# Optimization experiments

Hardware: AMD Instinct MI355X
Metric: run time of the kernel (lower is better)

The kernel has to match this reference:

```python
import jax, jax.numpy as jnp
import numpy as np

N_NODES = 50000
N_EDGES = 800000
D = 128
ALPHA = 0.2  # LeakyReLU negative slope


def setup_inputs() -> dict:
    key = jax.random.key(0)
    k1, k2, k3, k4 = jax.random.split(key, 4)
    inputs = jax.random.normal(k1, (N_NODES, D), dtype=jnp.float32)
    edge = jax.random.randint(k2, (2, N_EDGES), 0, N_NODES, dtype=jnp.int64)
    # xavier_normal with gain=1.414 as in the torch module
    std_W = 1.414 * np.sqrt(2.0 / (D + D))
    W = jax.random.normal(k3, (D, D), dtype=jnp.float32) * std_W
    std_a = 1.414 * np.sqrt(2.0 / (1 + D))
    a = jax.random.normal(k4, (1, D), dtype=jnp.float32) * std_a
    return {"inputs": inputs, "edge": edge, "W": W, "a": a}


def reference(inputs, edge, W, a):
    # h = inputs @ W  (shared projection; note concat([W,W],0) applied to
    # [x_src || x_dst] is exactly h[src] + h[dst])
    h = inputs @ W                                   # [N, D]
    src, dst = edge[0], edge[1]
    s = h[src] + h[dst]                              # [E, D] gathered edge features
    s = jnp.where(s > 0, s, ALPHA * s)               # LeakyReLU
    edge_e = jnp.exp(s @ a[0])                       # [E] unnormalized attention
    n = inputs.shape[0]
    # sparse.mm(coo, ones) -> per-row sum of edge_e; duplicates summed (coalesce)
    e_rowsum = jax.ops.segment_sum(edge_e, src, num_segments=n)        # [N]
    # sparse.mm(coo, h) -> sum_j edge_e * h[dst]
    h_prime = jax.ops.segment_sum(edge_e[:, None] * h[dst], src, num_segments=n)  # [N, D]
    h_prime = h_prime / e_rowsum[:, None]
    return jax.nn.relu(h_prime)  # concat=True path
```

## Files before the change

### kernel.cpp

```cpp
#include <hip/hip_runtime.h>
#include <cstdint>
#include <cstddef>

#define D 128
#define ALPHA 0.2f

typedef _Float16 half8_t __attribute__((ext_vector_type(8)));
typedef _Float16 v2h __attribute__((ext_vector_type(2)));
typedef __attribute__((ext_vector_type(4))) float f32x4_t;

static __device__ __forceinline__ ushort f2h(float f) {
    _Float16 h = (_Float16)f;
    return *(ushort*)&h;
}

static __device__ __forceinline__ float dot2f(v2h x, v2h y, float c) {
#if __has_builtin(__builtin_amdgcn_fdot2)
    return __builtin_amdgcn_fdot2(x, y, c, false);
#else
    return fmaf((float)x[0], (float)y[0], fmaf((float)x[1], (float)y[1], c));
#endif
}

__global__ __launch_bounds__(256) void prep_kernel(const float* __restrict__ W,
                                                   const float* __restrict__ a,
                                                   ushort* __restrict__ Wt,
                                                   ushort* __restrict__ Ah,
                                                   int* __restrict__ counts, int N) {
    int idx = blockIdx.x * 256 + threadIdx.x;
    if (idx < 16384) {
        int k = idx >> 7;
        int n = idx & 127;
        Wt[n * 128 + k] = f2h(W[idx]);
    }
    if (idx < 128) Ah[idx] = f2h(a[idx]);
    if (idx < N) counts[idx] = 0;
}

__global__ __launch_bounds__(256) void gemm_h_kernel(const float* __restrict__ A,
                                                     const ushort* __restrict__ Wt,
                                                     ushort* __restrict__ Hf,
                                                     int N) {
    __shared__ ushort Alds[64][136];
    const int tid = threadIdx.x;
    const int r0 = blockIdx.x * 64;

#pragma unroll
    for (int it = 0; it < 8; ++it) {
        int idx = it * 256 + tid;
        int r = idx >> 5;
        int c4 = (idx & 31) * 4;
        float4 v = make_float4(0.f, 0.f, 0.f, 0.f);
        if (r0 + r < N) v = *(const float4*)(A + (size_t)(r0 + r) * D + c4);
        ushort4 b;
        b.x = f2h(v.x); b.y = f2h(v.y); b.z = f2h(v.z); b.w = f2h(v.w);
        *(ushort4*)&Alds[r][c4] = b;
    }
    __syncthreads();

    const int lane = tid & 63;
    const int w = tid >> 6;
    const int wm = w >> 1;
    const int wn = w & 1;
    const int l15 = lane & 15;
    const int koff = (lane >> 4) * 8;

    f32x4_t acc[2][4];
#pragma unroll
    for (int mt = 0; mt < 2; ++mt)
#pragma unroll
        for (int nt = 0; nt < 4; ++nt) acc[mt][nt] = (f32x4_t){0.f, 0.f, 0.f, 0.f};

    const int arow = wm * 32 + l15;
#pragma unroll
    for (int kk = 0; kk < 4; ++kk) {
        half8_t am0 = *(const half8_t*)&Alds[arow][kk * 32 + koff];
        half8_t am1 = *(const half8_t*)&Alds[arow + 16][kk * 32 + koff];
        half8_t bn[4];
#pragma unroll
        for (int nt = 0; nt < 4; ++nt)
            bn[nt] = *(const half8_t*)(Wt + (size_t)(wn * 64 + nt * 16 + l15) * 128 + kk * 32 + koff);
#pragma unroll
        for (int nt = 0; nt < 4; ++nt) {
            acc[0][nt] = __builtin_amdgcn_mfma_f32_16x16x32_f16(am0, bn[nt], acc[0][nt], 0, 0, 0);
            acc[1][nt] = __builtin_amdgcn_mfma_f32_16x16x32_f16(am1, bn[nt], acc[1][nt], 0, 0, 0);
        }
    }

    const int crow = (lane >> 4) * 4;
#pragma unroll
    for (int mt = 0; mt < 2; ++mt)
#pragma unroll
        for (int nt = 0; nt < 4; ++nt)
#pragma unroll
            for (int r = 0; r < 4; ++r) {
                int row = r0 + wm * 32 + mt * 16 + crow + r;
                if (row < N)
                    Hf[(size_t)row * D + wn * 64 + nt * 16 + l15] = f2h(acc[mt][nt][r]);
            }
}

__global__ __launch_bounds__(256) void hist_rank_kernel(const int* __restrict__ src,
                                                        int* __restrict__ counts,
                                                        int* __restrict__ rank, int E) {
    int i = blockIdx.x * 256 + threadIdx.x;
    if (i >= E) return;
    rank[i] = atomicAdd(&counts[src[i]], 1);
}

__global__ __launch_bounds__(256) void scan_partial_kernel(const int* __restrict__ counts,
                                                           int* __restrict__ blocksum, int N) {
    __shared__ int wsum[4];
    int tid = threadIdx.x;
    int i = blockIdx.x * 256 + tid;
    int x = (i < N) ? counts[i] : 0;
#pragma unroll
    for (int off = 32; off > 0; off >>= 1) x += __shfl_down(x, off);
    if ((tid & 63) == 0) wsum[tid >> 6] = x;
    __syncthreads();
    if (tid == 0) blocksum[blockIdx.x] = wsum[0] + wsum[1] + wsum[2] + wsum[3];
}

__global__ __launch_bounds__(256) void scan_final_kernel(const int* __restrict__ counts,
                                                         const int* __restrict__ blocksum,
                                                         int* __restrict__ starts,
                                                         int nblk, int N) {
    __shared__ int bsum[4];
    __shared__ int wsum[4];
    int tid = threadIdx.x;
    int lane = tid & 63, w = tid >> 6;

    int x0 = (tid < nblk && tid < (int)blockIdx.x) ? blocksum[tid] : 0;
#pragma unroll
    for (int off = 32; off > 0; off >>= 1) x0 += __shfl_down(x0, off);
    if (lane == 0) bsum[w] = x0;
    __syncthreads();
    int blkoff = bsum[0] + bsum[1] + bsum[2] + bsum[3];

    int i = blockIdx.x * 256 + tid;
    int c = (i < N) ? counts[i] : 0;
    int x = c;
#pragma unroll
    for (int off = 1; off < 64; off <<= 1) {
        int y = __shfl_up(x, off);
        if (lane >= off) x += y;
    }
    if (lane == 63) wsum[w] = x;
    __syncthreads();
    int woff = blkoff;
    for (int j = 0; j < w; ++j) woff += wsum[j];
    int pre = woff + x - c;
    if (i < N) {
        starts[i] = pre;
        if (i == N - 1) starts[N] = pre + c;
    }
}

__global__ __launch_bounds__(256) void scatter_kernel(const int* __restrict__ src,
                                                      const int* __restrict__ dst,
                                                      const int* __restrict__ rank,
                                                      const int* __restrict__ starts,
                                                      int* __restrict__ dsts_sorted, int E) {
    int i = blockIdx.x * 256 + threadIdx.x;
    if (i >= E) return;
    int pos = starts[src[i]] + rank[i];
    dsts_sorted[pos] = dst[i];
}

template <bool FULL>
__device__ __forceinline__ void process_chunk(const ushort* __restrict__ Hf,
                                              const int* __restrict__ dsts_sorted,
                                              int base, int cnt, int l,
                                              v2h hs2, v2h av2, v2h alpha2,
                                              float& acc0, float& acc1, float& rsp) {
    uint fu[16];
#pragma unroll
    for (int j = 0; j < 16; ++j) {
        int idx = FULL ? (base + j) : (base + (j < cnt ? j : 0));
        int dj = dsts_sorted[idx];
        const ushort* rp = Hf + ((size_t)(uint)dj << 7);
        fu[j] = *(const uint*)(rp + (l << 1));
    }
    float p[16];
#pragma unroll
    for (int j = 0; j < 16; ++j) {
        v2h hv = *(v2h*)&fu[j];
        v2h s = hs2 + hv;
        s = __builtin_elementwise_max(s, s * alpha2);
        float pj = dot2f(s, av2, 0.0f);
        p[j] = (FULL || j < cnt) ? pj : -1e30f;
    }
    {
        bool hi = l & 1;
#pragma unroll
        for (int i = 0; i < 8; ++i) {
            float send = hi ? p[i] : p[i + 8];
            float recv = __shfl_xor(send, 1);
            p[i] = (hi ? p[i + 8] : p[i]) + recv;
        }
        hi = l & 2;
#pragma unroll
        for (int i = 0; i < 4; ++i) {
            float send = hi ? p[i] : p[i + 4];
            float recv = __shfl_xor(send, 2);
            p[i] = (hi ? p[i + 4] : p[i]) + recv;
        }
        hi = l & 4;
#pragma unroll
        for (int i = 0; i < 2; ++i) {
            float send = hi ? p[i] : p[i + 2];
            float recv = __shfl_xor(send, 4);
            p[i] = (hi ? p[i + 2] : p[i]) + recv;
        }
        hi = l & 8;
        {
            float send = hi ? p[0] : p[1];
            float recv = __shfl_xor(send, 8);
            p[0] = (hi ? p[1] : p[0]) + recv;
        }
        p[0] += __shfl_xor(p[0], 16);
        p[0] += __shfl_xor(p[0], 32);
    }
    float e = __expf(p[0]);
    rsp += e;

    const int brev[16] = {0, 8, 4, 12, 2, 10, 6, 14, 1, 9, 5, 13, 3, 11, 7, 15};
#pragma unroll
    for (int j = 0; j < 16; ++j) {
        float ej = __uint_as_float(
            (uint)__builtin_amdgcn_readlane((int)__float_as_uint(e), brev[j]));
        v2h hv = *(v2h*)&fu[j];
        acc0 = fmaf((float)hv[0], ej, acc0);
        acc1 = fmaf((float)hv[1], ej, acc1);
    }
}

__global__ __launch_bounds__(64) void node_kernel(const ushort* __restrict__ Hf,
                                                  const int* __restrict__ starts,
                                                  const int* __restrict__ dsts_sorted,
                                                  const ushort* __restrict__ Ah,
                                                  float* __restrict__ out, int N) {
    const int node = blockIdx.x;
    const int l = threadIdx.x;

    const int beg = starts[node];
    const int end = starts[node + 1];

    uint hu = *(const uint*)(Hf + ((size_t)node << 7) + (l << 1));
    v2h hs2 = *(v2h*)&hu;
    uint au = *(const uint*)(Ah + (l << 1));
    v2h av2 = *(v2h*)&au;
    const v2h alpha2 = {(_Float16)ALPHA, (_Float16)ALPHA};

    float acc0 = 0.f, acc1 = 0.f, rsp = 0.f;

    int base = beg;
    for (; base + 16 <= end; base += 16)
        process_chunk<true>(Hf, dsts_sorted, base, 16, l, hs2, av2, alpha2, acc0, acc1, rsp);
    if (base < end)
        process_chunk<false>(Hf, dsts_sorted, base, end - base, l, hs2, av2, alpha2, acc0, acc1, rsp);

    float rs = rsp;
    rs += __shfl_xor(rs, 1);
    rs += __shfl_xor(rs, 2);
    rs += __shfl_xor(rs, 4);
    rs += __shfl_xor(rs, 8);

    float inv = 1.0f / rs;
    float2 o;
    o.x = fmaxf(acc0 * inv, 0.f);
    o.y = fmaxf(acc1 * inv, 0.f);
    *(float2*)(out + ((size_t)node << 7) + (l << 1)) = o;
}

extern "C" void kernel_launch(void* const* d_in, const int* in_sizes, int n_in,
                              void* d_out, int out_size, void* d_ws, size_t ws_size,
                              hipStream_t stream) {
    const float* inputs = (const float*)d_in[0];
    const int* edge = (const int*)d_in[1];
    const float* W = (const float*)d_in[2];
    const float* a = (const float*)d_in[3];
    float* out = (float*)d_out;

    const int N = in_sizes[0] / D;
    const int E = in_sizes[1] / 2;

    const int* src = edge;
    const int* dst = edge + E;

    ushort* wt = (ushort*)d_ws;
    ushort* ah = wt + 16384;
    ushort* hf = ah + 128;
    int* counts = (int*)(hf + (size_t)N * D);
    int* starts = counts + N;
    int* blocksum = starts + N + 1;
    int* rank = blocksum + 256;
    int* dsts_sorted = rank + E;

    const int nblk = (N + 255) / 256;
    const int eblk = (E + 255) / 256;

    prep_kernel<<<nblk, 256, 0, stream>>>(W, a, wt, ah, counts, N);
    gemm_h_kernel<<<(N + 63) / 64, 256, 0, stream>>>(inputs, wt, hf, N);
    hist_rank_kernel<<<eblk, 256, 0, stream>>>(src, counts, rank, E);
    scan_partial_kernel<<<nblk, 256, 0, stream>>>(counts, blocksum, N);
    scan_final_kernel<<<nblk, 256, 0, stream>>>(counts, blocksum, starts, nblk, N);
    scatter_kernel<<<eblk, 256, 0, stream>>>(src, dst, rank, starts, dsts_sorted, E);
    node_kernel<<<N, 64, 0, stream>>>(hf, starts, dsts_sorted, ah, out, N);
}
```

Before: 116.7 us.

## Merge scan passes, fold zeroing into GEMM, and double-load neighbor chunks

Several changes land together. The two-pass block scan becomes a single kernel where each block re-sums all earlier counts directly. Zeroing the counts array moves into the GEMM kernel, and the 'a' conversion moves into the node kernel, which shrinks the prep kernel to W only. The node kernel now issues loads for two 16-edge chunks before computing either, raising memory-level parallelism on the gathers at the cost of more registers. The single-pass scan does quadratic total reads of counts (about 196 blocks each reading up to 50K ints), which costs bandwidth but saves one launch.

```diff
diff --git a/kernel.cpp b/kernel.cpp
--- a/kernel.cpp
+++ b/kernel.cpp
@@ -22,25 +22,22 @@
 #endif
 }
 
-__global__ __launch_bounds__(256) void prep_kernel(const float* __restrict__ W,
-                                                   const float* __restrict__ a,
-                                                   ushort* __restrict__ Wt,
-                                                   ushort* __restrict__ Ah,
-                                                   int* __restrict__ counts, int N) {
+__global__ __launch_bounds__(256) void w_prep_kernel(const float* __restrict__ W,
+                                                     ushort* __restrict__ Wt) {
     int idx = blockIdx.x * 256 + threadIdx.x;
-    if (idx < 16384) {
-        int k = idx >> 7;
-        int n = idx & 127;
-        Wt[n * 128 + k] = f2h(W[idx]);
-    }
-    if (idx < 128) Ah[idx] = f2h(a[idx]);
-    if (idx < N) counts[idx] = 0;
+    int k = idx >> 7;
+    int n = idx & 127;
+    Wt[n * 128 + k] = f2h(W[idx]);
 }
 
 __global__ __launch_bounds__(256) void gemm_h_kernel(const float* __restrict__ A,
                                                      const ushort* __restrict__ Wt,
                                                      ushort* __restrict__ Hf,
+                                                     int* __restrict__ counts,
                                                      int N) {
+    int zi = blockIdx.x * 256 + threadIdx.x;
+    if (zi < N) counts[zi] = 0;
+
     __shared__ ushort Alds[64][136];
     const int tid = threadIdx.x;
     const int r0 = blockIdx.x * 64;
@@ -108,36 +105,23 @@
     rank[i] = atomicAdd(&counts[src[i]], 1);
 }
 
-__global__ __launch_bounds__(256) void scan_partial_kernel(const int* __restrict__ counts,
-                                                           int* __restrict__ blocksum, int N) {
-    __shared__ int wsum[4];
-    int tid = threadIdx.x;
-    int i = blockIdx.x * 256 + tid;
-    int x = (i < N) ? counts[i] : 0;
-#pragma unroll
-    for (int off = 32; off > 0; off >>= 1) x += __shfl_down(x, off);
-    if ((tid & 63) == 0) wsum[tid >> 6] = x;
-    __syncthreads();
-    if (tid == 0) blocksum[blockIdx.x] = wsum[0] + wsum[1] + wsum[2] + wsum[3];
-}
-
-__global__ __launch_bounds__(256) void scan_final_kernel(const int* __restrict__ counts,
-                                                         const int* __restrict__ blocksum,
-                                                         int* __restrict__ starts,
-                                                         int nblk, int N) {
+__global__ __launch_bounds__(256) void scan_kernel(const int* __restrict__ counts,
+                                                   int* __restrict__ starts, int N) {
     __shared__ int bsum[4];
     __shared__ int wsum[4];
     int tid = threadIdx.x;
     int lane = tid & 63, w = tid >> 6;
 
-    int x0 = (tid < nblk && tid < (int)blockIdx.x) ? blocksum[tid] : 0;
+    int lim = blockIdx.x << 8;
+    int x0 = 0;
+    for (int i = tid; i < lim; i += 256) x0 += counts[i];
 #pragma unroll
     for (int off = 32; off > 0; off >>= 1) x0 += __shfl_down(x0, off);
     if (lane == 0) bsum[w] = x0;
     __syncthreads();
     int blkoff = bsum[0] + bsum[1] + bsum[2] + bsum[3];
 
-    int i = blockIdx.x * 256 + tid;
+    int i = (blockIdx.x << 8) + tid;
     int c = (i < N) ? counts[i] : 0;
     int x = c;
 #pragma unroll
@@ -167,20 +151,21 @@
     dsts_sorted[pos] = dst[i];
 }
 
-template <bool FULL>
-__device__ __forceinline__ void process_chunk(const ushort* __restrict__ Hf,
-                                              const int* __restrict__ dsts_sorted,
-                                              int base, int cnt, int l,
-                                              v2h hs2, v2h av2, v2h alpha2,
-                                              float& acc0, float& acc1, float& rsp) {
-    uint fu[16];
+__device__ __forceinline__ void load_chunk16(const ushort* __restrict__ Hf,
+                                             const int* __restrict__ dsts_sorted,
+                                             int base, int l, uint fu[16]) {
 #pragma unroll
     for (int j = 0; j < 16; ++j) {
-        int idx = FULL ? (base + j) : (base + (j < cnt ? j : 0));
-        int dj = dsts_sorted[idx];
+        int dj = dsts_sorted[base + j];
         const ushort* rp = Hf + ((size_t)(uint)dj << 7);
         fu[j] = *(const uint*)(rp + (l << 1));
     }
+}
+
+template <bool FULL>
+__device__ __forceinline__ void compute_chunk16(const uint fu[16], int cnt, int l,
+                                                v2h hs2, v2h av2, v2h alpha2,
+                                                float& acc0, float& acc1, float& rsp) {
     float p[16];
 #pragma unroll
     for (int j = 0; j < 16; ++j) {
@@ -238,7 +223,7 @@
 __global__ __launch_bounds__(64) void node_kernel(const ushort* __restrict__ Hf,
                                                   const int* __restrict__ starts,
                                                   const int* __restrict__ dsts_sorted,
-                                                  const ushort* __restrict__ Ah,
+                                                  const float* __restrict__ a,
                                                   float* __restrict__ out, int N) {
     const int node = blockIdx.x;
     const int l = threadIdx.x;
@@ -248,17 +233,37 @@
 
     uint hu = *(const uint*)(Hf + ((size_t)node << 7) + (l << 1));
     v2h hs2 = *(v2h*)&hu;
-    uint au = *(const uint*)(Ah + (l << 1));
-    v2h av2 = *(v2h*)&au;
+    float2 af = ((const float2*)a)[l];
+    v2h av2 = {(_Float16)af.x, (_Float16)af.y};
     const v2h alpha2 = {(_Float16)ALPHA, (_Float16)ALPHA};
 
     float acc0 = 0.f, acc1 = 0.f, rsp = 0.f;
 
     int base = beg;
-    for (; base + 16 <= end; base += 16)
-        process_chunk<true>(Hf, dsts_sorted, base, 16, l, hs2, av2, alpha2, acc0, acc1, rsp);
-    if (base < end)
-        process_chunk<false>(Hf, dsts_sorted, base, end - base, l, hs2, av2, alpha2, acc0, acc1, rsp);
+    for (; base + 32 <= end; base += 32) {
+        uint fuA[16], fuB[16];
+        load_chunk16(Hf, dsts_sorted, base, l, fuA);
+        load_chunk16(Hf, dsts_sorted, base + 16, l, fuB);
+        compute_chunk16<true>(fuA, 16, l, hs2, av2, alpha2, acc0, acc1, rsp);
+        compute_chunk16<true>(fuB, 16, l, hs2, av2, alpha2, acc0, acc1, rsp);
+    }
+    if (base + 16 <= end) {
+        uint fu[16];
+        load_chunk16(Hf, dsts_sorted, base, l, fu);
+        compute_chunk16<true>(fu, 16, l, hs2, av2, alpha2, acc0, acc1, rsp);
+        base += 16;
+    }
+    if (base < end) {
+        int cnt = end - base;
+        uint fu[16];
+#pragma unroll
+        for (int j = 0; j < 16; ++j) {
+            int dj = dsts_sorted[base + (j < cnt ? j : 0)];
+            const ushort* rp = Hf + ((size_t)(uint)dj << 7);
+            fu[j] = *(const uint*)(rp + (l << 1));
+        }
+        compute_chunk16<false>(fu, cnt, l, hs2, av2, alpha2, acc0, acc1, rsp);
+    }
 
     float rs = rsp;
     rs += __shfl_xor(rs, 1);
@@ -289,22 +294,19 @@
     const int* dst = edge + E;
 
     ushort* wt = (ushort*)d_ws;
-    ushort* ah = wt + 16384;
-    ushort* hf = ah + 128;
+    ushort* hf = wt + 16384;
     int* counts = (int*)(hf + (size_t)N * D);
     int* starts = counts + N;
-    int* blocksum = starts + N + 1;
-    int* rank = blocksum + 256;
+    int* rank = starts + N + 1;
     int* dsts_sorted = rank + E;
 
     const int nblk = (N + 255) / 256;
     const int eblk = (E + 255) / 256;
 
-    prep_kernel<<<nblk, 256, 0, stream>>>(W, a, wt, ah, counts, N);
-    gemm_h_kernel<<<(N + 63) / 64, 256, 0, stream>>>(inputs, wt, hf, N);
+    w_prep_kernel<<<64, 256, 0, stream>>>(W, wt);
+    gemm_h_kernel<<<(N + 63) / 64, 256, 0, stream>>>(inputs, wt, hf, counts, N);
     hist_rank_kernel<<<eblk, 256, 0, stream>>>(src, counts, rank, E);
-    scan_partial_kernel<<<nblk, 256, 0, stream>>>(counts, blocksum, N);
-    scan_final_kernel<<<nblk, 256, 0, stream>>>(counts, blocksum, starts, nblk, N);
+    scan_kernel<<<nblk, 256, 0, stream>>>(counts, starts, N);
     scatter_kernel<<<eblk, 256, 0, stream>>>(src, dst, rank, starts, dsts_sorted, E);
-    node_kernel<<<N, 64, 0, stream>>>(hf, starts, dsts_sorted, ah, out, N);
-}
+    node_kernel<<<N, 64, 0, stream>>>(hf, starts, dsts_sorted, a, out, N);
+}
```

Result: slower. 147.5 us (+26.3%).

## Partition histogram and scatter by source range; use atomic cursors instead of rank array

Applied to the files above, without the earlier changes.

The histogram and scatter kernels now launch eight times as many blocks, and each group handles only edges whose source falls in one eighth of the node range. The apparent aim is to keep atomic targets local to one XCD/L2 slice. The per-edge rank array is dropped: the scatter kernel takes slots with atomic increments on a cursor array initialised from the scan. In exchange, every edge is read eight times in both kernels, and neighbour order within a row is no longer deterministic.

```diff
diff --git a/kernel.cpp b/kernel.cpp
--- a/kernel.cpp
+++ b/kernel.cpp
@@ -100,12 +100,17 @@
             }
 }
 
-__global__ __launch_bounds__(256) void hist_rank_kernel(const int* __restrict__ src,
-                                                        int* __restrict__ counts,
-                                                        int* __restrict__ rank, int E) {
-    int i = blockIdx.x * 256 + threadIdx.x;
+__global__ __launch_bounds__(256) void hist8_kernel(const int* __restrict__ src,
+                                                    int* __restrict__ counts,
+                                                    int E, int N) {
+    int b = blockIdx.x;
+    int g = b & 7;
+    int i = ((b >> 3) << 8) + threadIdx.x;
     if (i >= E) return;
-    rank[i] = atomicAdd(&counts[src[i]], 1);
+    int s = src[i];
+    int lo = (g * N) >> 3;
+    int hi = ((g + 1) * N) >> 3;
+    if (s >= lo && s < hi) atomicAdd(&counts[s], 1);
 }
 
 __global__ __launch_bounds__(256) void scan_partial_kernel(const int* __restrict__ counts,
@@ -124,6 +129,7 @@
 __global__ __launch_bounds__(256) void scan_final_kernel(const int* __restrict__ counts,
                                                          const int* __restrict__ blocksum,
                                                          int* __restrict__ starts,
+                                                         int* __restrict__ cursor,
                                                          int nblk, int N) {
     __shared__ int bsum[4];
     __shared__ int wsum[4];
@@ -152,19 +158,27 @@
     int pre = woff + x - c;
     if (i < N) {
         starts[i] = pre;
+        cursor[i] = pre;
         if (i == N - 1) starts[N] = pre + c;
     }
 }
 
-__global__ __launch_bounds__(256) void scatter_kernel(const int* __restrict__ src,
-                                                      const int* __restrict__ dst,
-                                                      const int* __restrict__ rank,
-                                                      const int* __restrict__ starts,
-                                                      int* __restrict__ dsts_sorted, int E) {
-    int i = blockIdx.x * 256 + threadIdx.x;
+__global__ __launch_bounds__(256) void scatter8_kernel(const int* __restrict__ src,
+                                                       const int* __restrict__ dst,
+                                                       int* __restrict__ cursor,
+                                                       int* __restrict__ dsts_sorted,
+                                                       int E, int N) {
+    int b = blockIdx.x;
+    int g = b & 7;
+    int i = ((b >> 3) << 8) + threadIdx.x;
     if (i >= E) return;
-    int pos = starts[src[i]] + rank[i];
-    dsts_sorted[pos] = dst[i];
+    int s = src[i];
+    int lo = (g * N) >> 3;
+    int hi = ((g + 1) * N) >> 3;
+    if (s >= lo && s < hi) {
+        int pos = atomicAdd(&cursor[s], 1);
+        dsts_sorted[pos] = dst[i];
+    }
 }
 
 template <bool FULL>
@@ -293,18 +307,18 @@
     ushort* hf = ah + 128;
     int* counts = (int*)(hf + (size_t)N * D);
     int* starts = counts + N;
-    int* blocksum = starts + N + 1;
-    int* rank = blocksum + 256;
-    int* dsts_sorted = rank + E;
+    int* cursor = starts + N + 1;
+    int* blocksum = cursor + N;
+    int* dsts_sorted = blocksum + 256;
 
     const int nblk = (N + 255) / 256;
     const int eblk = (E + 255) / 256;
 
     prep_kernel<<<nblk, 256, 0, stream>>>(W, a, wt, ah, counts, N);
     gemm_h_kernel<<<(N + 63) / 64, 256, 0, stream>>>(inputs, wt, hf, N);
-    hist_rank_kernel<<<eblk, 256, 0, stream>>>(src, counts, rank, E);
+    hist8_kernel<<<8 * eblk, 256, 0, stream>>>(src, counts, E, N);
     scan_partial_kernel<<<nblk, 256, 0, stream>>>(counts, blocksum, N);
-    scan_final_kernel<<<nblk, 256, 0, stream>>>(counts, blocksum, starts, nblk, N);
-    scatter_kernel<<<eblk, 256, 0, stream>>>(src, dst, rank, starts, dsts_sorted, E);
+    scan_final_kernel<<<nblk, 256, 0, stream>>>(counts, blocksum, starts, cursor, nblk, N);
+    scatter8_kernel<<<8 * eblk, 256, 0, stream>>>(src, dst, cursor, dsts_sorted, E, N);
     node_kernel<<<N, 64, 0, stream>>>(hf, starts, dsts_sorted, ah, out, N);
 }
```

Result: slower. 141.7 us (+21.4%).
